# Kernel optimization log

Hardware: AMD Instinct MI355X
Metric: run time of the kernel (lower is better)

Reference implementation:

```python
import jax, jax.numpy as jnp
import numpy as np

N_NODES = 50000
N_EDGES = 500000
N_GRAPHS = 512


def _segmean(vals, ids, num):
    # avg aggregation: segment mean with safe divide for empty segments
    s = jax.ops.segment_sum(vals, ids, num_segments=num)
    c = jax.ops.segment_sum(jnp.ones((vals.shape[0], 1), vals.dtype), ids, num_segments=num)
    return s / jnp.maximum(c, 1.0)


def setup_inputs() -> dict:
    key = jax.random.key(0)
    ks = iter(jax.random.split(key, 64))

    def nrm(shape, scale=0.05):
        return jax.random.normal(next(ks), shape, dtype=jnp.float32) * scale

    inp = {}
    inp['x'] = nrm((N_NODES, 64), 1.0)
    inp['e'] = nrm((N_EDGES, 32), 1.0)
    inp['u'] = nrm((N_GRAPHS, 64), 1.0)
    inp['a'] = nrm((N_GRAPHS, 8), 1.0)
    inp['senders'] = jax.random.randint(next(ks), (N_EDGES,), 0, N_NODES)
    inp['receivers'] = jax.random.randint(next(ks), (N_EDGES,), 0, N_NODES)
    inp['node_graph'] = jnp.sort(jax.random.randint(next(ks), (N_NODES,), 0, N_GRAPHS))
    inp['edge_graph'] = jnp.sort(jax.random.randint(next(ks), (N_EDGES,), 0, N_GRAPHS))
    # block 1 (hidden 256)
    inp['We1'] = nrm((32, 256)); inp['be1'] = jnp.zeros((256,), jnp.float32)
    inp['Wn1'] = nrm((64, 256)); inp['Win1'] = nrm((256, 256)); inp['Wout1'] = nrm((256, 256)); inp['bn1'] = jnp.zeros((256,), jnp.float32)
    inp['Wg1'] = nrm((64, 256)); inp['Wgn1'] = nrm((256, 256)); inp['Wge1'] = nrm((256, 256)); inp['bg1'] = jnp.zeros((256,), jnp.float32)
    # block 2 (hidden 128)
    inp['We2'] = nrm((256, 128)); inp['be2'] = jnp.zeros((128,), jnp.float32)
    inp['Wn2'] = nrm((256, 128)); inp['Win2'] = nrm((128, 128)); inp['Wout2'] = nrm((128, 128)); inp['bn2'] = jnp.zeros((128,), jnp.float32)
    inp['Wg2'] = nrm((256, 128)); inp['Wgn2'] = nrm((128, 128)); inp['Wge2'] = nrm((128, 128)); inp['bg2'] = jnp.zeros((128,), jnp.float32)
    # global readout (global_features only)
    inp['Wga'] = nrm((128, 128)); inp['bga'] = jnp.zeros((128,), jnp.float32)
    # action-value MLP: (128 + 8) -> 256 -> 256 -> 1
    inp['Wa1'] = nrm((136, 256)); inp['ba1'] = jnp.zeros((256,), jnp.float32)
    inp['Wa2'] = nrm((256, 256)); inp['ba2'] = jnp.zeros((256,), jnp.float32)
    inp['Wa3'] = nrm((256, 1)); inp['ba3'] = jnp.zeros((1,), jnp.float32)
    return inp


def reference(x, e, u, a, senders, receivers, node_graph, edge_graph,
              We1, be1, Wn1, Win1, Wout1, bn1, Wg1, Wgn1, Wge1, bg1,
              We2, be2, Wn2, Win2, Wout2, bn2, Wg2, Wgn2, Wge2, bg2,
              Wga, bga, Wa1, ba1, Wa2, ba2, Wa3, ba3):
    # --- GraphNetwork block 1 (hidden 256) ---
    e1 = jax.nn.relu(e @ We1 + be1)                                  # [E,256]
    inc1 = _segmean(e1, receivers, N_NODES)                          # avg incoming per node
    out1 = _segmean(e1, senders, N_NODES)                            # avg outgoing per node
    n1 = jax.nn.relu(x @ Wn1 + inc1 @ Win1 + out1 @ Wout1 + bn1)     # [N,256]
    u1 = jax.nn.relu(u @ Wg1 + _segmean(n1, node_graph, N_GRAPHS) @ Wgn1
                     + _segmean(e1, edge_graph, N_GRAPHS) @ Wge1 + bg1)  # [B,256]
    # --- GraphNetwork block 2 (hidden 128) ---
    e2 = jax.nn.relu(e1 @ We2 + be2)                                 # [E,128]
    inc2 = _segmean(e2, receivers, N_NODES)
    out2 = _segmean(e2, senders, N_NODES)
    n2 = jax.nn.relu(n1 @ Wn2 + inc2 @ Win2 + out2 @ Wout2 + bn2)    # [N,128]
    u2 = jax.nn.relu(u1 @ Wg2 + _segmean(n2, node_graph, N_GRAPHS) @ Wgn2
                     + _segmean(e2, edge_graph, N_GRAPHS) @ Wge2 + bg2)  # [B,128]
    # --- global readout + action-value MLP ---
    state_value = u2 @ Wga + bga                                     # [B,128]
    h = jnp.concatenate([state_value, a], axis=1)                    # [B,136]
    h = jax.nn.relu(h @ Wa1 + ba1)
    h = jax.nn.relu(h @ Wa2 + ba2)
    return h @ Wa3 + ba3                                             # [B,1]
```

## Files before the change

### kernel.cpp

```cpp
#include <hip/hip_runtime.h>
#include <hip/hip_bf16.h>

#define N_NODES 50000
#define N_EDGES 500000
#define N_GRAPHS 512

#define FXS16 2048.0f
#define FXI16 4.8828125e-4f

__device__ __forceinline__ unsigned long long pk16x4(float4 v) {
    const unsigned long long a = (unsigned int)fmaf(v.x, FXS16, 0.5f);
    const unsigned long long b = (unsigned int)fmaf(v.y, FXS16, 0.5f);
    const unsigned long long c = (unsigned int)fmaf(v.z, FXS16, 0.5f);
    const unsigned long long d = (unsigned int)fmaf(v.w, FXS16, 0.5f);
    return a | (b << 16) | (c << 32) | (d << 48);
}

typedef __attribute__((ext_vector_type(8))) short bf16x8;
typedef __attribute__((ext_vector_type(4))) float f32x4;

__global__ __launch_bounds__(256) void prep_kernel(
    const float* __restrict__ We2,  const float* __restrict__ Wn1,
    const float* __restrict__ Win1, const float* __restrict__ Wout1,
    const float* __restrict__ Wn2,  const float* __restrict__ Win2,
    const float* __restrict__ Wout2,
    __hip_bfloat16* __restrict__ Wt2,  __hip_bfloat16* __restrict__ Wn1t,
    __hip_bfloat16* __restrict__ Win1t,__hip_bfloat16* __restrict__ Wout1t,
    __hip_bfloat16* __restrict__ Wn2t, __hip_bfloat16* __restrict__ Win2t,
    __hip_bfloat16* __restrict__ Wout2t)
{
    const int b = blockIdx.x, t = threadIdx.x;
    const float* src; __hip_bfloat16* dst; int K, N, base;
    if (b < 128)      { src = We2;   dst = Wt2;    K = 256; N = 128; base = 0; }
    else if (b < 192) { src = Wn1;   dst = Wn1t;   K = 64;  N = 256; base = 128; }
    else if (b < 448) { src = Win1;  dst = Win1t;  K = 256; N = 256; base = 192; }
    else if (b < 704) { src = Wout1; dst = Wout1t; K = 256; N = 256; base = 448; }
    else if (b < 832) { src = Wn2;   dst = Wn2t;   K = 256; N = 128; base = 704; }
    else if (b < 896) { src = Win2;  dst = Win2t;  K = 128; N = 128; base = 832; }
    else              { src = Wout2; dst = Wout2t; K = 128; N = 128; base = 896; }
    const int i = (b - base) * 256 + t;
    const int n = i / K, k = i - n * K;
    dst[i] = __float2bfloat16(src[(size_t)k * N + n]);
}

#define EPB 32
#define E1P 264
#define E2P 132

__global__ __launch_bounds__(256) void edge_kernel(
    const float* __restrict__ e,
    const int* __restrict__ senders,
    const int* __restrict__ receivers,
    const int* __restrict__ edge_graph,
    const float* __restrict__ We1, const float* __restrict__ be1,
    const __hip_bfloat16* __restrict__ Wt2,
    const float* __restrict__ be2,
    unsigned long long* __restrict__ inc1u, unsigned long long* __restrict__ out1u,
    unsigned long long* __restrict__ inc2u, unsigned long long* __restrict__ out2u,
    float* __restrict__ rcnt, float* __restrict__ scnt,
    float* __restrict__ ge1, float* __restrict__ ge2, float* __restrict__ gecnt)
{
    __shared__ float eL[EPB * 32];
    __shared__ __hip_bfloat16 e1B[EPB * E1P];
    __shared__ float e2L[EPB * E2P];
    __shared__ int ridx[EPB], sidx[EPB], gidx[EPB];

    const int t = threadIdx.x;
    const long e0 = (long)blockIdx.x * EPB;

    for (int i = t; i < EPB * 32; i += 256) eL[i] = e[e0 * 32 + i];
    if (t < EPB) {
        ridx[t] = receivers[e0 + t];
        sidx[t] = senders[e0 + t];
        gidx[t] = edge_graph[e0 + t];
    }
    __syncthreads();

    {
        const int c0 = (t & 63) * 4;
        const int jb = (t >> 6) * 8;
        float4 acc[8];
        const float4 b4 = *(const float4*)&be1[c0];
        #pragma unroll
        for (int j = 0; j < 8; j++) acc[j] = b4;
        for (int k = 0; k < 32; k += 4) {
            float4 v[8];
            #pragma unroll
            for (int j = 0; j < 8; j++) v[j] = *(const float4*)&eL[(jb + j) * 32 + k];
            #pragma unroll
            for (int kk = 0; kk < 4; kk++) {
                const float4 w = *(const float4*)&We1[(size_t)(k + kk) * 256 + c0];
                #pragma unroll
                for (int j = 0; j < 8; j++) {
                    const float vv = ((const float*)&v[j])[kk];
                    acc[j].x = fmaf(vv, w.x, acc[j].x);
                    acc[j].y = fmaf(vv, w.y, acc[j].y);
                    acc[j].z = fmaf(vv, w.z, acc[j].z);
                    acc[j].w = fmaf(vv, w.w, acc[j].w);
                }
            }
        }
        #pragma unroll
        for (int j = 0; j < 8; j++) {
            const float2 p0 = make_float2(fmaxf(acc[j].x, 0.f), fmaxf(acc[j].y, 0.f));
            const float2 p1 = make_float2(fmaxf(acc[j].z, 0.f), fmaxf(acc[j].w, 0.f));
            *(__hip_bfloat162*)&e1B[(jb + j) * E1P + c0]     = __float22bfloat162_rn(p0);
            *(__hip_bfloat162*)&e1B[(jb + j) * E1P + c0 + 2] = __float22bfloat162_rn(p1);
        }
    }
    __syncthreads();

    {
        const int wv = t >> 6, ln = t & 63;
        const int r0 = ln & 15, q = ln >> 4;
        f32x4 acc[2][2] = {{{0.f,0.f,0.f,0.f},{0.f,0.f,0.f,0.f}},
                           {{0.f,0.f,0.f,0.f},{0.f,0.f,0.f,0.f}}};
        const int n0 = (2 * wv) * 16 + r0;
        const int n1 = (2 * wv + 1) * 16 + r0;
        #pragma unroll
        for (int kb = 0; kb < 8; kb++) {
            const int k0 = kb * 32 + q * 8;
            const bf16x8 a0 = *(const bf16x8*)&e1B[(r0) * E1P + k0];
            const bf16x8 a1 = *(const bf16x8*)&e1B[(16 + r0) * E1P + k0];
            const bf16x8 b0 = *(const bf16x8*)&Wt2[(size_t)n0 * 256 + k0];
            const bf16x8 b1 = *(const bf16x8*)&Wt2[(size_t)n1 * 256 + k0];
            acc[0][0] = __builtin_amdgcn_mfma_f32_16x16x32_bf16(a0, b0, acc[0][0], 0, 0, 0);
            acc[0][1] = __builtin_amdgcn_mfma_f32_16x16x32_bf16(a0, b1, acc[0][1], 0, 0, 0);
            acc[1][0] = __builtin_amdgcn_mfma_f32_16x16x32_bf16(a1, b0, acc[1][0], 0, 0, 0);
            acc[1][1] = __builtin_amdgcn_mfma_f32_16x16x32_bf16(a1, b1, acc[1][1], 0, 0, 0);
        }
        const float bz0 = be2[2 * wv * 16 + r0];
        const float bz1 = be2[(2 * wv + 1) * 16 + r0];
        #pragma unroll
        for (int mt = 0; mt < 2; mt++) {
            const int m = mt * 16 + q * 4;
            #pragma unroll
            for (int r = 0; r < 4; r++) {
                e2L[(m + r) * E2P + 2 * wv * 16 + r0]       = fmaxf(acc[mt][0][r] + bz0, 0.f);
                e2L[(m + r) * E2P + (2 * wv + 1) * 16 + r0] = fmaxf(acc[mt][1][r] + bz1, 0.f);
            }
        }
    }
    __syncthreads();

    {
        const int w = t & 63;
        const int ep = (t >> 6) & 1;
        unsigned long long* arr = (t < 128) ? inc1u : out1u;
        const int* idx = (t < 128) ? ridx : sidx;
        #pragma unroll
        for (int jj = 0; jj < EPB / 2; jj++) {
            const int j = jj * 2 + ep;
            const float2 v0 = __bfloat1622float2(*(const __hip_bfloat162*)&e1B[j * E1P + 4 * w]);
            const float2 v1 = __bfloat1622float2(*(const __hip_bfloat162*)&e1B[j * E1P + 4 * w + 2]);
            float4 v; v.x = v0.x; v.y = v0.y; v.z = v1.x; v.w = v1.y;
            atomicAdd(&arr[(size_t)idx[j] * 64 + w], pk16x4(v));
        }
    }
    {
        const int w = t & 31;
        const int eq = (t >> 5) & 3;
        unsigned long long* arr = (t < 128) ? inc2u : out2u;
        const int* idx = (t < 128) ? ridx : sidx;
        #pragma unroll
        for (int jj = 0; jj < EPB / 4; jj++) {
            const int j = jj * 4 + eq;
            const float4 v = *(const float4*)&e2L[j * E2P + 4 * w];
            atomicAdd(&arr[(size_t)idx[j] * 32 + w], pk16x4(v));
        }
    }
    if (gidx[0] == gidx[EPB - 1]) {
        const int g = gidx[0];
        float s = 0.f;
        #pragma unroll
        for (int j = 0; j < EPB; j++) s += __bfloat162float(e1B[j * E1P + t]);
        atomicAdd(&ge1[(size_t)g * 256 + t], s);
        if (t < 128) {
            float s2 = 0.f;
            #pragma unroll
            for (int j = 0; j < EPB; j++) s2 += e2L[j * E2P + t];
            atomicAdd(&ge2[(size_t)g * 128 + t], s2);
        }
        if (t == 0) atomicAdd(&gecnt[g], (float)EPB);
    } else {
        int j = 0;
        while (j < EPB) {
            const int g = gidx[j];
            int j2 = j;
            float s = 0.f;
            while (j2 < EPB && gidx[j2] == g) { s += __bfloat162float(e1B[j2 * E1P + t]); j2++; }
            atomicAdd(&ge1[(size_t)g * 256 + t], s);
            if (t < 128) {
                float s2 = 0.f;
                for (int jj = j; jj < j2; jj++) s2 += e2L[jj * E2P + t];
                atomicAdd(&ge2[(size_t)g * 128 + t], s2);
            }
            if (t == 0) atomicAdd(&gecnt[g], (float)(j2 - j));
            j = j2;
        }
    }
    if (t < EPB) {
        atomicAdd(&rcnt[ridx[t]], 1.f);
        atomicAdd(&scnt[sidx[t]], 1.f);
    }
}

#define NPB 16
#define XP  72
#define K1P 264
#define K2P 136

__global__ __launch_bounds__(256) void node_kernel(
    const float* __restrict__ x,
    const int* __restrict__ node_graph,
    const unsigned long long* __restrict__ inc1u, const unsigned long long* __restrict__ out1u,
    const unsigned long long* __restrict__ inc2u, const unsigned long long* __restrict__ out2u,
    const float* __restrict__ rcnt, const float* __restrict__ scnt,
    const __hip_bfloat16* __restrict__ Wn1t, const __hip_bfloat16* __restrict__ Win1t,
    const __hip_bfloat16* __restrict__ Wout1t, const float* __restrict__ bn1,
    const __hip_bfloat16* __restrict__ Wn2t, const __hip_bfloat16* __restrict__ Win2t,
    const __hip_bfloat16* __restrict__ Wout2t, const float* __restrict__ bn2,
    float* __restrict__ gn1, float* __restrict__ gn2, float* __restrict__ gncnt)
{
    __shared__ __hip_bfloat16 xB[NPB * XP];
    __shared__ __hip_bfloat16 i1B[NPB * K1P];
    __shared__ __hip_bfloat16 o1B[NPB * K1P];
    __shared__ __hip_bfloat16 i2B[NPB * K2P];
    __shared__ __hip_bfloat16 o2B[NPB * K2P];
    __shared__ __hip_bfloat16 n1B[NPB * K1P];
    __shared__ __hip_bfloat16 n2B[NPB * K2P];
    __shared__ int gI[NPB];
    __shared__ float rrcp[NPB], srcp[NPB];

    const int t = threadIdx.x;
    const long n0 = (long)blockIdx.x * NPB;

    if (t < NPB) {
        gI[t] = node_graph[n0 + t];
        rrcp[t] = FXI16 / fmaxf(rcnt[n0 + t], 1.f);
        srcp[t] = FXI16 / fmaxf(scnt[n0 + t], 1.f);
    }
    for (int i = t; i < NPB * 16; i += 256) {
        const int j = i >> 4, c4 = (i & 15) * 4;
        const float4 v = *(const float4*)&x[(n0 + j) * 64 + c4];
        *(__hip_bfloat162*)&xB[j * XP + c4]     = __float22bfloat162_rn(make_float2(v.x, v.y));
        *(__hip_bfloat162*)&xB[j * XP + c4 + 2] = __float22bfloat162_rn(make_float2(v.z, v.w));
    }
    __syncthreads();

    for (int i = t; i < NPB * 64; i += 256) {
        const int j = i >> 6, w = i & 63;
        const size_t n = (size_t)(n0 + j);
        const unsigned long long av = inc1u[n * 64 + w];
        const unsigned long long bv = out1u[n * 64 + w];
        const float rr = rrcp[j], sr = srcp[j];
        const float2 a01 = make_float2((float)(unsigned int)(av & 0xFFFF) * rr,
                                       (float)(unsigned int)((av >> 16) & 0xFFFF) * rr);
        const float2 a23 = make_float2((float)(unsigned int)((av >> 32) & 0xFFFF) * rr,
                                       (float)(unsigned int)(av >> 48) * rr);
        const float2 b01 = make_float2((float)(unsigned int)(bv & 0xFFFF) * sr,
                                       (float)(unsigned int)((bv >> 16) & 0xFFFF) * sr);
        const float2 b23 = make_float2((float)(unsigned int)((bv >> 32) & 0xFFFF) * sr,
                                       (float)(unsigned int)(bv >> 48) * sr);
        *(__hip_bfloat162*)&i1B[j * K1P + 4 * w]     = __float22bfloat162_rn(a01);
        *(__hip_bfloat162*)&i1B[j * K1P + 4 * w + 2] = __float22bfloat162_rn(a23);
        *(__hip_bfloat162*)&o1B[j * K1P + 4 * w]     = __float22bfloat162_rn(b01);
        *(__hip_bfloat162*)&o1B[j * K1P + 4 * w + 2] = __float22bfloat162_rn(b23);
    }
    for (int i = t; i < NPB * 32; i += 256) {
        const int j = i >> 5, w = i & 31;
        const size_t n = (size_t)(n0 + j);
        const unsigned long long av = inc2u[n * 32 + w];
        const unsigned long long bv = out2u[n * 32 + w];
        const float rr = rrcp[j], sr = srcp[j];
        const float2 a01 = make_float2((float)(unsigned int)(av & 0xFFFF) * rr,
                                       (float)(unsigned int)((av >> 16) & 0xFFFF) * rr);
        const float2 a23 = make_float2((float)(unsigned int)((av >> 32) & 0xFFFF) * rr,
                                       (float)(unsigned int)(av >> 48) * rr);
        const float2 b01 = make_float2((float)(unsigned int)(bv & 0xFFFF) * sr,
                                       (float)(unsigned int)((bv >> 16) & 0xFFFF) * sr);
        const float2 b23 = make_float2((float)(unsigned int)((bv >> 32) & 0xFFFF) * sr,
                                       (float)(unsigned int)(bv >> 48) * sr);
        *(__hip_bfloat162*)&i2B[j * K2P + 4 * w]     = __float22bfloat162_rn(a01);
        *(__hip_bfloat162*)&i2B[j * K2P + 4 * w + 2] = __float22bfloat162_rn(a23);
        *(__hip_bfloat162*)&o2B[j * K2P + 4 * w]     = __float22bfloat162_rn(b01);
        *(__hip_bfloat162*)&o2B[j * K2P + 4 * w + 2] = __float22bfloat162_rn(b23);
    }
    __syncthreads();

    const int wv = t >> 6, ln = t & 63;
    const int r0 = ln & 15, q = ln >> 4;

    {
        f32x4 acc[4] = {{0.f,0.f,0.f,0.f},{0.f,0.f,0.f,0.f},
                        {0.f,0.f,0.f,0.f},{0.f,0.f,0.f,0.f}};
        #pragma unroll
        for (int ks = 0; ks < 2; ks++) {
            const int k0 = ks * 32 + q * 8;
            const bf16x8 a = *(const bf16x8*)&xB[r0 * XP + k0];
            #pragma unroll
            for (int nn = 0; nn < 4; nn++) {
                const int n = (wv * 4 + nn) * 16 + r0;
                const bf16x8 b = *(const bf16x8*)&Wn1t[(size_t)n * 64 + k0];
                acc[nn] = __builtin_amdgcn_mfma_f32_16x16x32_bf16(a, b, acc[nn], 0, 0, 0);
            }
        }
        #pragma unroll
        for (int ks = 0; ks < 8; ks++) {
            const int k0 = ks * 32 + q * 8;
            const bf16x8 a = *(const bf16x8*)&i1B[r0 * K1P + k0];
            #pragma unroll
            for (int nn = 0; nn < 4; nn++) {
                const int n = (wv * 4 + nn) * 16 + r0;
                const bf16x8 b = *(const bf16x8*)&Win1t[(size_t)n * 256 + k0];
                acc[nn] = __builtin_amdgcn_mfma_f32_16x16x32_bf16(a, b, acc[nn], 0, 0, 0);
            }
        }
        #pragma unroll
        for (int ks = 0; ks < 8; ks++) {
            const int k0 = ks * 32 + q * 8;
            const bf16x8 a = *(const bf16x8*)&o1B[r0 * K1P + k0];
            #pragma unroll
            for (int nn = 0; nn < 4; nn++) {
                const int n = (wv * 4 + nn) * 16 + r0;
                const bf16x8 b = *(const bf16x8*)&Wout1t[(size_t)n * 256 + k0];
                acc[nn] = __builtin_amdgcn_mfma_f32_16x16x32_bf16(a, b, acc[nn], 0, 0, 0);
            }
        }
        #pragma unroll
        for (int nn = 0; nn < 4; nn++) {
            const int n = (wv * 4 + nn) * 16 + r0;
            const float bz = bn1[n];
            #pragma unroll
            for (int r = 0; r < 4; r++) {
                const int m = q * 4 + r;
                n1B[m * K1P + n] = __float2bfloat16(fmaxf(acc[nn][r] + bz, 0.f));
            }
        }
    }
    __syncthreads();

    if (gI[0] == gI[NPB - 1]) {
        float s = 0.f;
        #pragma unroll
        for (int j = 0; j < NPB; j++) s += __bfloat162float(n1B[j * K1P + t]);
        atomicAdd(&gn1[(size_t)gI[0] * 256 + t], s);
        if (t == 0) atomicAdd(&gncnt[gI[0]], (float)NPB);
    } else {
        int j = 0;
        while (j < NPB) {
            const int g = gI[j];
            int j2 = j;
            float s = 0.f;
            while (j2 < NPB && gI[j2] == g) { s += __bfloat162float(n1B[j2 * K1P + t]); j2++; }
            atomicAdd(&gn1[(size_t)g * 256 + t], s);
            if (t == 0) atomicAdd(&gncnt[g], (float)(j2 - j));
            j = j2;
        }
    }

    {
        f32x4 acc[2] = {{0.f,0.f,0.f,0.f},{0.f,0.f,0.f,0.f}};
        #pragma unroll
        for (int ks = 0; ks < 8; ks++) {
            const int k0 = ks * 32 + q * 8;
            const bf16x8 a = *(const bf16x8*)&n1B[r0 * K1P + k0];
            #pragma unroll
            for (int nn = 0; nn < 2; nn++) {
                const int n = (wv * 2 + nn) * 16 + r0;
                const bf16x8 b = *(const bf16x8*)&Wn2t[(size_t)n * 256 + k0];
                acc[nn] = __builtin_amdgcn_mfma_f32_16x16x32_bf16(a, b, acc[nn], 0, 0, 0);
            }
        }
        #pragma unroll
        for (int ks = 0; ks < 4; ks++) {
            const int k0 = ks * 32 + q * 8;
            const bf16x8 a = *(const bf16x8*)&i2B[r0 * K2P + k0];
            #pragma unroll
            for (int nn = 0; nn < 2; nn++) {
                const int n = (wv * 2 + nn) * 16 + r0;
                const bf16x8 b = *(const bf16x8*)&Win2t[(size_t)n * 128 + k0];
                acc[nn] = __builtin_amdgcn_mfma_f32_16x16x32_bf16(a, b, acc[nn], 0, 0, 0);
            }
        }
        #pragma unroll
        for (int ks = 0; ks < 4; ks++) {
            const int k0 = ks * 32 + q * 8;
            const bf16x8 a = *(const bf16x8*)&o2B[r0 * K2P + k0];
            #pragma unroll
            for (int nn = 0; nn < 2; nn++) {
                const int n = (wv * 2 + nn) * 16 + r0;
                const bf16x8 b = *(const bf16x8*)&Wout2t[(size_t)n * 128 + k0];
                acc[nn] = __builtin_amdgcn_mfma_f32_16x16x32_bf16(a, b, acc[nn], 0, 0, 0);
            }
        }
        #pragma unroll
        for (int nn = 0; nn < 2; nn++) {
            const int n = (wv * 2 + nn) * 16 + r0;
            const float bz = bn2[n];
            #pragma unroll
            for (int r = 0; r < 4; r++) {
                const int m = q * 4 + r;
                n2B[m * K2P + n] = __float2bfloat16(fmaxf(acc[nn][r] + bz, 0.f));
            }
        }
    }
    __syncthreads();

    if (t < 128) {
        if (gI[0] == gI[NPB - 1]) {
            float s = 0.f;
            #pragma unroll
            for (int j = 0; j < NPB; j++) s += __bfloat162float(n2B[j * K2P + t]);
            atomicAdd(&gn2[(size_t)gI[0] * 128 + t], s);
        } else {
            int j = 0;
            while (j < NPB) {
                const int g = gI[j];
                int j2 = j;
                float s = 0.f;
                while (j2 < NPB && gI[j2] == g) { s += __bfloat162float(n2B[j2 * K2P + t]); j2++; }
                atomicAdd(&gn2[(size_t)g * 128 + t], s);
                j = j2;
            }
        }
    }
}

__global__ __launch_bounds__(256) void graph_kernel(
    const float* __restrict__ u,
    const float* __restrict__ a,
    const float* __restrict__ ge1, const float* __restrict__ ge2,
    const float* __restrict__ gecnt,
    const float* __restrict__ gn1, const float* __restrict__ gn2,
    const float* __restrict__ gncnt,
    const float* __restrict__ Wg1, const float* __restrict__ Wgn1,
    const float* __restrict__ Wge1, const float* __restrict__ bg1,
    const float* __restrict__ Wg2, const float* __restrict__ Wgn2,
    const float* __restrict__ Wge2, const float* __restrict__ bg2,
    const float* __restrict__ Wga, const float* __restrict__ bga,
    const float* __restrict__ Wa1, const float* __restrict__ ba1,
    const float* __restrict__ Wa2, const float* __restrict__ ba2,
    const float* __restrict__ Wa3, const float* __restrict__ ba3,
    float* __restrict__ out)
{
    const int g = blockIdx.x;
    const int t = threadIdx.x;
    __shared__ float uL[64], mn1[256], me1[256], mn2[128], me2[128];
    __shared__ float u1L[256], u2L[128], hL[144], h1L[256], h2L[256];
    __shared__ float red[4];

    const float ec = 1.f / fmaxf(gecnt[g], 1.f);
    const float nc = 1.f / fmaxf(gncnt[g], 1.f);
    if (t < 64) uL[t] = u[(size_t)g * 64 + t];
    mn1[t] = gn1[(size_t)g * 256 + t] * nc;
    me1[t] = ge1[(size_t)g * 256 + t] * ec;
    if (t < 128) {
        mn2[t] = gn2[(size_t)g * 128 + t] * nc;
        me2[t] = ge2[(size_t)g * 128 + t] * ec;
    }
    if (t >= 136 && t < 144) hL[t] = 0.f;
    __syncthreads();

    {
        float acc = bg1[t];
        for (int k = 0; k < 64; k++)  acc = fmaf(uL[k],  Wg1[(size_t)k * 256 + t], acc);
        for (int k = 0; k < 256; k++) acc = fmaf(mn1[k], Wgn1[(size_t)k * 256 + t], acc);
        for (int k = 0; k < 256; k++) acc = fmaf(me1[k], Wge1[(size_t)k * 256 + t], acc);
        u1L[t] = fmaxf(acc, 0.f);
    }
    __syncthreads();
    if (t < 128) {
        float acc = bg2[t];
        for (int k = 0; k < 256; k++) acc = fmaf(u1L[k], Wg2[(size_t)k * 128 + t], acc);
        for (int k = 0; k < 128; k++) acc = fmaf(mn2[k], Wgn2[(size_t)k * 128 + t], acc);
        for (int k = 0; k < 128; k++) acc = fmaf(me2[k], Wge2[(size_t)k * 128 + t], acc);
        u2L[t] = fmaxf(acc, 0.f);
    }
    __syncthreads();
    if (t < 128) {
        float acc = bga[t];
        for (int k = 0; k < 128; k++) acc = fmaf(u2L[k], Wga[(size_t)k * 128 + t], acc);
        hL[t] = acc;
    }
    if (t >= 128 && t < 136) hL[t] = a[(size_t)g * 8 + (t - 128)];
    __syncthreads();
    {
        float acc = ba1[t];
        for (int k = 0; k < 136; k++) acc = fmaf(hL[k], Wa1[(size_t)k * 256 + t], acc);
        h1L[t] = fmaxf(acc, 0.f);
    }
    __syncthreads();
    {
        float acc = ba2[t];
        for (int k = 0; k < 256; k++) acc = fmaf(h1L[k], Wa2[(size_t)k * 256 + t], acc);
        h2L[t] = fmaxf(acc, 0.f);
    }
    __syncthreads();
    {
        float p = h2L[t] * Wa3[t];
        for (int off = 32; off > 0; off >>= 1) p += __shfl_down(p, off, 64);
        if ((t & 63) == 0) red[t >> 6] = p;
        __syncthreads();
        if (t == 0) out[g] = red[0] + red[1] + red[2] + red[3] + ba3[0];
    }
}

extern "C" void kernel_launch(void* const* d_in, const int* in_sizes, int n_in,
                              void* d_out, int out_size, void* d_ws, size_t ws_size,
                              hipStream_t stream) {
    const float* x          = (const float*)d_in[0];
    const float* e          = (const float*)d_in[1];
    const float* u          = (const float*)d_in[2];
    const float* a          = (const float*)d_in[3];
    const int*   senders    = (const int*)d_in[4];
    const int*   receivers  = (const int*)d_in[5];
    const int*   node_graph = (const int*)d_in[6];
    const int*   edge_graph = (const int*)d_in[7];
    const float* We1 = (const float*)d_in[8];  const float* be1 = (const float*)d_in[9];
    const float* Wn1 = (const float*)d_in[10]; const float* Win1 = (const float*)d_in[11];
    const float* Wout1 = (const float*)d_in[12]; const float* bn1 = (const float*)d_in[13];
    const float* Wg1 = (const float*)d_in[14]; const float* Wgn1 = (const float*)d_in[15];
    const float* Wge1 = (const float*)d_in[16]; const float* bg1 = (const float*)d_in[17];
    const float* We2 = (const float*)d_in[18]; const float* be2 = (const float*)d_in[19];
    const float* Wn2 = (const float*)d_in[20]; const float* Win2 = (const float*)d_in[21];
    const float* Wout2 = (const float*)d_in[22]; const float* bn2 = (const float*)d_in[23];
    const float* Wg2 = (const float*)d_in[24]; const float* Wgn2 = (const float*)d_in[25];
    const float* Wge2 = (const float*)d_in[26]; const float* bg2 = (const float*)d_in[27];
    const float* Wga = (const float*)d_in[28]; const float* bga = (const float*)d_in[29];
    const float* Wa1 = (const float*)d_in[30]; const float* ba1 = (const float*)d_in[31];
    const float* Wa2 = (const float*)d_in[32]; const float* ba2 = (const float*)d_in[33];
    const float* Wa3 = (const float*)d_in[34]; const float* ba3 = (const float*)d_in[35];

    unsigned long long* uw = (unsigned long long*)d_ws;
    unsigned long long* inc1u = uw;                       uw += (size_t)N_NODES * 64;
    unsigned long long* out1u = uw;                       uw += (size_t)N_NODES * 64;
    unsigned long long* inc2u = uw;                       uw += (size_t)N_NODES * 32;
    unsigned long long* out2u = uw;                       uw += (size_t)N_NODES * 32;
    float* fw = (float*)uw;
    float* rcnt = fw;  fw += N_NODES;
    float* scnt = fw;  fw += N_NODES;
    float* ge1  = fw;  fw += (size_t)N_GRAPHS * 256;
    float* ge2  = fw;  fw += (size_t)N_GRAPHS * 128;
    float* gecnt = fw; fw += N_GRAPHS;
    float* gn1  = fw;  fw += (size_t)N_GRAPHS * 256;
    float* gn2  = fw;  fw += (size_t)N_GRAPHS * 128;
    float* gncnt = fw; fw += N_GRAPHS;
    const size_t total_bytes = (char*)fw - (char*)d_ws;
    __hip_bfloat16* bw = (__hip_bfloat16*)fw;
    __hip_bfloat16* Wt2    = bw;  bw += 128 * 256;
    __hip_bfloat16* Wn1t   = bw;  bw += 256 * 64;
    __hip_bfloat16* Win1t  = bw;  bw += 256 * 256;
    __hip_bfloat16* Wout1t = bw;  bw += 256 * 256;
    __hip_bfloat16* Wn2t   = bw;  bw += 128 * 256;
    __hip_bfloat16* Win2t  = bw;  bw += 128 * 128;
    __hip_bfloat16* Wout2t = bw;  bw += 128 * 128;

    hipMemsetAsync(d_ws, 0, total_bytes, stream);

    prep_kernel<<<960, 256, 0, stream>>>(
        We2, Wn1, Win1, Wout1, Wn2, Win2, Wout2,
        Wt2, Wn1t, Win1t, Wout1t, Wn2t, Win2t, Wout2t);

    edge_kernel<<<N_EDGES / EPB, 256, 0, stream>>>(
        e, senders, receivers, edge_graph, We1, be1, Wt2, be2,
        inc1u, out1u, inc2u, out2u, rcnt, scnt, ge1, ge2, gecnt);

    node_kernel<<<N_NODES / NPB, 256, 0, stream>>>(
        x, node_graph, inc1u, out1u, inc2u, out2u, rcnt, scnt,
        Wn1t, Win1t, Wout1t, bn1, Wn2t, Win2t, Wout2t, bn2, gn1, gn2, gncnt);

    graph_kernel<<<N_GRAPHS, 256, 0, stream>>>(
        u, a, ge1, ge2, gecnt, gn1, gn2, gncnt,
        Wg1, Wgn1, Wge1, bg1, Wg2, Wgn2, Wge2, bg2,
        Wga, bga, Wa1, ba1, Wa2, ba2, Wa3, ba3, (float*)d_out);
}
```

Baseline: 1.041 ms.

## Replace atomic scatter aggregation with CSR gather for node means

Builds CSR adjacency for receivers and senders on the device every call (count, scan, fill). The edge kernel then writes per-edge e1 (bf16) and e2 (fixed-point u16) to buffers instead of atomically scattering them into per-node accumulators. The node kernel gathers each node's incoming and outgoing edges through the CSR lists and computes the means before its MFMA GEMMs. This removes heavy 64-bit atomic contention, but adds several extra launches, about 384 MB of edge-feature buffer traffic, and random gathers. The new path runs only when the workspace is large enough, otherwise the old path is used.

```diff
diff --git a/kernel.cpp b/kernel.cpp
--- a/kernel.cpp
+++ b/kernel.cpp
@@ -43,9 +43,460 @@
     dst[i] = __float2bfloat16(src[(size_t)k * N + n]);
 }
 
+
+#define NTILES 196
+
+__global__ __launch_bounds__(256) void count_kernel(
+    const int* __restrict__ senders, const int* __restrict__ receivers,
+    unsigned int* __restrict__ rc, unsigned int* __restrict__ sc)
+{
+    const int i = blockIdx.x * 256 + threadIdx.x;
+    if (i < N_EDGES) {
+        atomicAdd(&rc[receivers[i]], 1u);
+        atomicAdd(&sc[senders[i]], 1u);
+    }
+}
+
+__global__ __launch_bounds__(256) void scan_tile_sum(
+    const unsigned int* __restrict__ rc, const unsigned int* __restrict__ sc,
+    unsigned int* __restrict__ tsR, unsigned int* __restrict__ tsS)
+{
+    const int b = blockIdx.x;
+    const int sel = (b >= NTILES);
+    const int tile = sel ? b - NTILES : b;
+    const unsigned int* src = sel ? sc : rc;
+    unsigned int* ts = sel ? tsS : tsR;
+    const int t = threadIdx.x;
+    const int i = tile * 256 + t;
+    unsigned int v = (i < N_NODES) ? src[i] : 0u;
+    __shared__ unsigned int s[256];
+    s[t] = v; __syncthreads();
+    for (int off = 128; off > 0; off >>= 1) {
+        if (t < off) s[t] += s[t + off];
+        __syncthreads();
+    }
+    if (t == 0) ts[tile] = s[0];
+}
+
+__global__ __launch_bounds__(256) void scan_tile_offsets(
+    unsigned int* __restrict__ tsR, unsigned int* __restrict__ tsS,
+    int* __restrict__ roff, int* __restrict__ soff)
+{
+    __shared__ unsigned int s[256];
+    const int t = threadIdx.x;
+    for (int sel = 0; sel < 2; sel++) {
+        unsigned int* ts = sel ? tsS : tsR;
+        int* off = sel ? soff : roff;
+        unsigned int v = (t < NTILES) ? ts[t] : 0u;
+        s[t] = v; __syncthreads();
+        for (int o = 1; o < 256; o <<= 1) {
+            unsigned int x = (t >= o) ? s[t - o] : 0u;
+            __syncthreads();
+            s[t] += x;
+            __syncthreads();
+        }
+        const unsigned int incl = s[t];
+        if (t < NTILES) ts[t] = incl - v;
+        if (t == NTILES - 1) off[N_NODES] = (int)incl;
+        __syncthreads();
+    }
+}
+
+__global__ __launch_bounds__(256) void scan_finalize(
+    const unsigned int* __restrict__ rc, const unsigned int* __restrict__ sc,
+    const unsigned int* __restrict__ tsR, const unsigned int* __restrict__ tsS,
+    int* __restrict__ roff, int* __restrict__ soff,
+    unsigned int* __restrict__ wpR, unsigned int* __restrict__ wpS)
+{
+    const int b = blockIdx.x;
+    const int sel = (b >= NTILES);
+    const int tile = sel ? b - NTILES : b;
+    const unsigned int* src = sel ? sc : rc;
+    const unsigned int* ts = sel ? tsS : tsR;
+    int* off = sel ? soff : roff;
+    unsigned int* wp = sel ? wpS : wpR;
+    const int t = threadIdx.x, i = tile * 256 + t;
+    unsigned int v = (i < N_NODES) ? src[i] : 0u;
+    __shared__ unsigned int s[256];
+    s[t] = v; __syncthreads();
+    for (int o = 1; o < 256; o <<= 1) {
+        unsigned int x = (t >= o) ? s[t - o] : 0u;
+        __syncthreads();
+        s[t] += x;
+        __syncthreads();
+    }
+    const unsigned int excl = s[t] - v + ts[tile];
+    if (i < N_NODES) { off[i] = (int)excl; wp[i] = excl; }
+}
+
+__global__ __launch_bounds__(256) void csr_fill(
+    const int* __restrict__ senders, const int* __restrict__ receivers,
+    unsigned int* __restrict__ wpR, unsigned int* __restrict__ wpS,
+    int* __restrict__ csrR, int* __restrict__ csrS)
+{
+    const int i = blockIdx.x * 256 + threadIdx.x;
+    if (i < N_EDGES) {
+        csrR[atomicAdd(&wpR[receivers[i]], 1u)] = i;
+        csrS[atomicAdd(&wpS[senders[i]], 1u)] = i;
+    }
+}
+
 #define EPB 32
 #define E1P 264
 #define E2P 132
+
+__global__ __launch_bounds__(256) void edge_kernel_csr(
+    const float* __restrict__ e,
+    const int* __restrict__ edge_graph,
+    const float* __restrict__ We1, const float* __restrict__ be1,
+    const __hip_bfloat16* __restrict__ Wt2,
+    const float* __restrict__ be2,
+    __hip_bfloat16* __restrict__ e1buf, unsigned short* __restrict__ e2buf,
+    float* __restrict__ ge1, float* __restrict__ ge2, float* __restrict__ gecnt)
+{
+    __shared__ float eL[EPB * 32];
+    __shared__ __hip_bfloat16 e1B[EPB * E1P];
+    __shared__ float e2L[EPB * E2P];
+    __shared__ int gidx[EPB];
+
+    const int t = threadIdx.x;
+    const long e0 = (long)blockIdx.x * EPB;
+
+    for (int i = t; i < EPB * 32; i += 256) eL[i] = e[e0 * 32 + i];
+    if (t < EPB) gidx[t] = edge_graph[e0 + t];
+    __syncthreads();
+
+    {
+        const int c0 = (t & 63) * 4;
+        const int jb = (t >> 6) * 8;
+        float4 acc[8];
+        const float4 b4 = *(const float4*)&be1[c0];
+        #pragma unroll
+        for (int j = 0; j < 8; j++) acc[j] = b4;
+        for (int k = 0; k < 32; k += 4) {
+            float4 v[8];
+            #pragma unroll
+            for (int j = 0; j < 8; j++) v[j] = *(const float4*)&eL[(jb + j) * 32 + k];
+            #pragma unroll
+            for (int kk = 0; kk < 4; kk++) {
+                const float4 w = *(const float4*)&We1[(size_t)(k + kk) * 256 + c0];
+                #pragma unroll
+                for (int j = 0; j < 8; j++) {
+                    const float vv = ((const float*)&v[j])[kk];
+                    acc[j].x = fmaf(vv, w.x, acc[j].x);
+                    acc[j].y = fmaf(vv, w.y, acc[j].y);
+                    acc[j].z = fmaf(vv, w.z, acc[j].z);
+                    acc[j].w = fmaf(vv, w.w, acc[j].w);
+                }
+            }
+        }
+        #pragma unroll
+        for (int j = 0; j < 8; j++) {
+            const float2 p0 = make_float2(fmaxf(acc[j].x, 0.f), fmaxf(acc[j].y, 0.f));
+            const float2 p1 = make_float2(fmaxf(acc[j].z, 0.f), fmaxf(acc[j].w, 0.f));
+            *(__hip_bfloat162*)&e1B[(jb + j) * E1P + c0]     = __float22bfloat162_rn(p0);
+            *(__hip_bfloat162*)&e1B[(jb + j) * E1P + c0 + 2] = __float22bfloat162_rn(p1);
+        }
+    }
+    __syncthreads();
+
+    {
+        const int wv = t >> 6, ln = t & 63;
+        const int r0 = ln & 15, q = ln >> 4;
+        f32x4 acc[2][2] = {{{0.f,0.f,0.f,0.f},{0.f,0.f,0.f,0.f}},
+                           {{0.f,0.f,0.f,0.f},{0.f,0.f,0.f,0.f}}};
+        const int n0 = (2 * wv) * 16 + r0;
+        const int n1 = (2 * wv + 1) * 16 + r0;
+        #pragma unroll
+        for (int kb = 0; kb < 8; kb++) {
+            const int k0 = kb * 32 + q * 8;
+            const bf16x8 a0 = *(const bf16x8*)&e1B[(r0) * E1P + k0];
+            const bf16x8 a1 = *(const bf16x8*)&e1B[(16 + r0) * E1P + k0];
+            const bf16x8 b0 = *(const bf16x8*)&Wt2[(size_t)n0 * 256 + k0];
+            const bf16x8 b1 = *(const bf16x8*)&Wt2[(size_t)n1 * 256 + k0];
+            acc[0][0] = __builtin_amdgcn_mfma_f32_16x16x32_bf16(a0, b0, acc[0][0], 0, 0, 0);
+            acc[0][1] = __builtin_amdgcn_mfma_f32_16x16x32_bf16(a0, b1, acc[0][1], 0, 0, 0);
+            acc[1][0] = __builtin_amdgcn_mfma_f32_16x16x32_bf16(a1, b0, acc[1][0], 0, 0, 0);
+            acc[1][1] = __builtin_amdgcn_mfma_f32_16x16x32_bf16(a1, b1, acc[1][1], 0, 0, 0);
+        }
+        const float bz0 = be2[2 * wv * 16 + r0];
+        const float bz1 = be2[(2 * wv + 1) * 16 + r0];
+        #pragma unroll
+        for (int mt = 0; mt < 2; mt++) {
+            const int m = mt * 16 + q * 4;
+            #pragma unroll
+            for (int r = 0; r < 4; r++) {
+                e2L[(m + r) * E2P + 2 * wv * 16 + r0]       = fmaxf(acc[mt][0][r] + bz0, 0.f);
+                e2L[(m + r) * E2P + (2 * wv + 1) * 16 + r0] = fmaxf(acc[mt][1][r] + bz1, 0.f);
+            }
+        }
+    }
+    __syncthreads();
+
+    for (int i = t; i < EPB * 32; i += 256) {
+        const int j = i >> 5, c8 = (i & 31) * 8;
+        *(bf16x8*)&e1buf[(size_t)(e0 + j) * 256 + c8] = *(const bf16x8*)&e1B[j * E1P + c8];
+    }
+    for (int i = t; i < EPB * 32; i += 256) {
+        const int j = i >> 5, c4 = (i & 31) * 4;
+        const float4 v = *(const float4*)&e2L[j * E2P + c4];
+        ushort4 pk;
+        pk.x = (unsigned short)fmaf(v.x, FXS16, 0.5f);
+        pk.y = (unsigned short)fmaf(v.y, FXS16, 0.5f);
+        pk.z = (unsigned short)fmaf(v.z, FXS16, 0.5f);
+        pk.w = (unsigned short)fmaf(v.w, FXS16, 0.5f);
+        *(ushort4*)&e2buf[(size_t)(e0 + j) * 128 + c4] = pk;
+    }
+
+    if (gidx[0] == gidx[EPB - 1]) {
+        const int g = gidx[0];
+        float s = 0.f;
+        #pragma unroll
+        for (int j = 0; j < EPB; j++) s += __bfloat162float(e1B[j * E1P + t]);
+        atomicAdd(&ge1[(size_t)g * 256 + t], s);
+        if (t < 128) {
+            float s2 = 0.f;
+            #pragma unroll
+            for (int j = 0; j < EPB; j++) s2 += e2L[j * E2P + t];
+            atomicAdd(&ge2[(size_t)g * 128 + t], s2);
+        }
+        if (t == 0) atomicAdd(&gecnt[g], (float)EPB);
+    } else {
+        int j = 0;
+        while (j < EPB) {
+            const int g = gidx[j];
+            int j2 = j;
+            float s = 0.f;
+            while (j2 < EPB && gidx[j2] == g) { s += __bfloat162float(e1B[j2 * E1P + t]); j2++; }
+            atomicAdd(&ge1[(size_t)g * 256 + t], s);
+            if (t < 128) {
+                float s2 = 0.f;
+                for (int jj = j; jj < j2; jj++) s2 += e2L[jj * E2P + t];
+                atomicAdd(&ge2[(size_t)g * 128 + t], s2);
+            }
+            if (t == 0) atomicAdd(&gecnt[g], (float)(j2 - j));
+            j = j2;
+        }
+    }
+}
+
+#define NPB 16
+#define XP  72
+#define K1P 264
+#define K2P 136
+
+__global__ __launch_bounds__(256) void node_kernel_csr(
+    const float* __restrict__ x,
+    const int* __restrict__ node_graph,
+    const int* __restrict__ roff, const int* __restrict__ soff,
+    const int* __restrict__ csrR, const int* __restrict__ csrS,
+    const __hip_bfloat16* __restrict__ e1buf, const unsigned short* __restrict__ e2buf,
+    const __hip_bfloat16* __restrict__ Wn1t, const __hip_bfloat16* __restrict__ Win1t,
+    const __hip_bfloat16* __restrict__ Wout1t, const float* __restrict__ bn1,
+    const __hip_bfloat16* __restrict__ Wn2t, const __hip_bfloat16* __restrict__ Win2t,
+    const __hip_bfloat16* __restrict__ Wout2t, const float* __restrict__ bn2,
+    float* __restrict__ gn1, float* __restrict__ gn2, float* __restrict__ gncnt)
+{
+    __shared__ __hip_bfloat16 xB[NPB * XP];
+    __shared__ __hip_bfloat16 i1B[NPB * K1P];
+    __shared__ __hip_bfloat16 o1B[NPB * K1P];
+    __shared__ __hip_bfloat16 i2B[NPB * K2P];
+    __shared__ __hip_bfloat16 o2B[NPB * K2P];
+    __shared__ __hip_bfloat16 n1B[NPB * K1P];
+    __shared__ __hip_bfloat16 n2B[NPB * K2P];
+    __shared__ int gI[NPB];
+
+    const int t = threadIdx.x;
+    const long n0 = (long)blockIdx.x * NPB;
+
+    if (t < NPB) gI[t] = node_graph[n0 + t];
+    for (int i = t; i < NPB * 16; i += 256) {
+        const int j = i >> 4, c4 = (i & 15) * 4;
+        const float4 v = *(const float4*)&x[(n0 + j) * 64 + c4];
+        *(__hip_bfloat162*)&xB[j * XP + c4]     = __float22bfloat162_rn(make_float2(v.x, v.y));
+        *(__hip_bfloat162*)&xB[j * XP + c4 + 2] = __float22bfloat162_rn(make_float2(v.z, v.w));
+    }
+
+    const int wv = t >> 6, ln = t & 63;
+    const int h = ln >> 5, l5 = ln & 31;
+    const int* off = h ? soff : roff;
+    const int* lst = h ? csrS : csrR;
+    __hip_bfloat16* d1 = h ? o1B : i1B;
+    __hip_bfloat16* d2 = h ? o2B : i2B;
+
+    for (int jj = 0; jj < 4; jj++) {
+        const int j = wv * 4 + jj;
+        const long node = n0 + j;
+        const int o = off[node], oE = off[node + 1];
+        float a1[8] = {0.f,0.f,0.f,0.f,0.f,0.f,0.f,0.f};
+        float a2[4] = {0.f,0.f,0.f,0.f};
+        int i = o;
+        int id = (i < oE) ? lst[i] : 0;
+        while (i < oE) {
+            const int idc = id;
+            ++i;
+            id = (i < oE) ? lst[i] : 0;
+            const bf16x8 r1 = *(const bf16x8*)&e1buf[(size_t)idc * 256 + l5 * 8];
+            const ushort4 r2 = *(const ushort4*)&e2buf[(size_t)idc * 128 + l5 * 4];
+            #pragma unroll
+            for (int c = 0; c < 8; c++)
+                a1[c] += __uint_as_float(((unsigned int)(unsigned short)r1[c]) << 16);
+            a2[0] += (float)r2.x; a2[1] += (float)r2.y;
+            a2[2] += (float)r2.z; a2[3] += (float)r2.w;
+        }
+        const int cnt = oE - o;
+        const float inv = 1.f / (float)(cnt > 0 ? cnt : 1);
+        const float inv2 = inv * FXI16;
+        #pragma unroll
+        for (int c = 0; c < 4; c++) {
+            *(__hip_bfloat162*)&d1[j * K1P + l5 * 8 + 2 * c] =
+                __float22bfloat162_rn(make_float2(a1[2 * c] * inv, a1[2 * c + 1] * inv));
+        }
+        *(__hip_bfloat162*)&d2[j * K2P + l5 * 4] =
+            __float22bfloat162_rn(make_float2(a2[0] * inv2, a2[1] * inv2));
+        *(__hip_bfloat162*)&d2[j * K2P + l5 * 4 + 2] =
+            __float22bfloat162_rn(make_float2(a2[2] * inv2, a2[3] * inv2));
+    }
+    __syncthreads();
+
+    const int r0 = ln & 15, q = ln >> 4;
+
+    {
+        f32x4 acc[4] = {{0.f,0.f,0.f,0.f},{0.f,0.f,0.f,0.f},
+                        {0.f,0.f,0.f,0.f},{0.f,0.f,0.f,0.f}};
+        #pragma unroll
+        for (int ks = 0; ks < 2; ks++) {
+            const int k0 = ks * 32 + q * 8;
+            const bf16x8 a = *(const bf16x8*)&xB[r0 * XP + k0];
+            #pragma unroll
+            for (int nn = 0; nn < 4; nn++) {
+                const int n = (wv * 4 + nn) * 16 + r0;
+                const bf16x8 b = *(const bf16x8*)&Wn1t[(size_t)n * 64 + k0];
+                acc[nn] = __builtin_amdgcn_mfma_f32_16x16x32_bf16(a, b, acc[nn], 0, 0, 0);
+            }
+        }
+        #pragma unroll
+        for (int ks = 0; ks < 8; ks++) {
+            const int k0 = ks * 32 + q * 8;
+            const bf16x8 a = *(const bf16x8*)&i1B[r0 * K1P + k0];
+            #pragma unroll
+            for (int nn = 0; nn < 4; nn++) {
+                const int n = (wv * 4 + nn) * 16 + r0;
+                const bf16x8 b = *(const bf16x8*)&Win1t[(size_t)n * 256 + k0];
+                acc[nn] = __builtin_amdgcn_mfma_f32_16x16x32_bf16(a, b, acc[nn], 0, 0, 0);
+            }
+        }
+        #pragma unroll
+        for (int ks = 0; ks < 8; ks++) {
+            const int k0 = ks * 32 + q * 8;
+            const bf16x8 a = *(const bf16x8*)&o1B[r0 * K1P + k0];
+            #pragma unroll
+            for (int nn = 0; nn < 4; nn++) {
+                const int n = (wv * 4 + nn) * 16 + r0;
+                const bf16x8 b = *(const bf16x8*)&Wout1t[(size_t)n * 256 + k0];
+                acc[nn] = __builtin_amdgcn_mfma_f32_16x16x32_bf16(a, b, acc[nn], 0, 0, 0);
+            }
+        }
+        #pragma unroll
+        for (int nn = 0; nn < 4; nn++) {
+            const int n = (wv * 4 + nn) * 16 + r0;
+            const float bz = bn1[n];
+            #pragma unroll
+            for (int r = 0; r < 4; r++) {
+                const int m = q * 4 + r;
+                n1B[m * K1P + n] = __float2bfloat16(fmaxf(acc[nn][r] + bz, 0.f));
+            }
+        }
+    }
+    __syncthreads();
+
+    if (gI[0] == gI[NPB - 1]) {
+        float s = 0.f;
+        #pragma unroll
+        for (int j = 0; j < NPB; j++) s += __bfloat162float(n1B[j * K1P + t]);
+        atomicAdd(&gn1[(size_t)gI[0] * 256 + t], s);
+        if (t == 0) atomicAdd(&gncnt[gI[0]], (float)NPB);
+    } else {
+        int j = 0;
+        while (j < NPB) {
+            const int g = gI[j];
+            int j2 = j;
+            float s = 0.f;
+            while (j2 < NPB && gI[j2] == g) { s += __bfloat162float(n1B[j2 * K1P + t]); j2++; }
+            atomicAdd(&gn1[(size_t)g * 256 + t], s);
+            if (t == 0) atomicAdd(&gncnt[g], (float)(j2 - j));
+            j = j2;
+        }
+    }
+
+    {
+        f32x4 acc[2] = {{0.f,0.f,0.f,0.f},{0.f,0.f,0.f,0.f}};
+        #pragma unroll
+        for (int ks = 0; ks < 8; ks++) {
+            const int k0 = ks * 32 + q * 8;
+            const bf16x8 a = *(const bf16x8*)&n1B[r0 * K1P + k0];
+            #pragma unroll
+            for (int nn = 0; nn < 2; nn++) {
+                const int n = (wv * 2 + nn) * 16 + r0;
+                const bf16x8 b = *(const bf16x8*)&Wn2t[(size_t)n * 256 + k0];
+                acc[nn] = __builtin_amdgcn_mfma_f32_16x16x32_bf16(a, b, acc[nn], 0, 0, 0);
+            }
+        }
+        #pragma unroll
+        for (int ks = 0; ks < 4; ks++) {
+            const int k0 = ks * 32 + q * 8;
+            const bf16x8 a = *(const bf16x8*)&i2B[r0 * K2P + k0];
+            #pragma unroll
+            for (int nn = 0; nn < 2; nn++) {
+                const int n = (wv * 2 + nn) * 16 + r0;
+                const bf16x8 b = *(const bf16x8*)&Win2t[(size_t)n * 128 + k0];
+                acc[nn] = __builtin_amdgcn_mfma_f32_16x16x32_bf16(a, b, acc[nn], 0, 0, 0);
+            }
+        }
+        #pragma unroll
+        for (int ks = 0; ks < 4; ks++) {
+            const int k0 = ks * 32 + q * 8;
+            const bf16x8 a = *(const bf16x8*)&o2B[r0 * K2P + k0];
+            #pragma unroll
+            for (int nn = 0; nn < 2; nn++) {
+                const int n = (wv * 2 + nn) * 16 + r0;
+                const bf16x8 b = *(const bf16x8*)&Wout2t[(size_t)n * 128 + k0];
+                acc[nn] = __builtin_amdgcn_mfma_f32_16x16x32_bf16(a, b, acc[nn], 0, 0, 0);
+            }
+        }
+        #pragma unroll
+        for (int nn = 0; nn < 2; nn++) {
+            const int n = (wv * 2 + nn) * 16 + r0;
+            const float bz = bn2[n];
+            #pragma unroll
+            for (int r = 0; r < 4; r++) {
+                const int m = q * 4 + r;
+                n2B[m * K2P + n] = __float2bfloat16(fmaxf(acc[nn][r] + bz, 0.f));
+            }
+        }
+    }
+    __syncthreads();
+
+    if (t < 128) {
+        if (gI[0] == gI[NPB - 1]) {
+            float s = 0.f;
+            #pragma unroll
+            for (int j = 0; j < NPB; j++) s += __bfloat162float(n2B[j * K2P + t]);
+            atomicAdd(&gn2[(size_t)gI[0] * 128 + t], s);
+        } else {
+            int j = 0;
+            while (j < NPB) {
+                const int g = gI[j];
+                int j2 = j;
+                float s = 0.f;
+                while (j2 < NPB && gI[j2] == g) { s += __bfloat162float(n2B[j2 * K2P + t]); j2++; }
+                atomicAdd(&gn2[(size_t)g * 128 + t], s);
+                j = j2;
+            }
+        }
+    }
+}
+
 
 __global__ __launch_bounds__(256) void edge_kernel(
     const float* __restrict__ e,
@@ -204,11 +655,6 @@
         atomicAdd(&scnt[sidx[t]], 1.f);
     }
 }
-
-#define NPB 16
-#define XP  72
-#define K1P 264
-#define K2P 136
 
 __global__ __launch_bounds__(256) void node_kernel(
     const float* __restrict__ x,
@@ -532,6 +978,72 @@
     const float* Wa2 = (const float*)d_in[32]; const float* ba2 = (const float*)d_in[33];
     const float* Wa3 = (const float*)d_in[34]; const float* ba3 = (const float*)d_in[35];
 
+    {
+        char* p = (char*)d_ws;
+        auto take = [&p](size_t bytes) {
+            char* q = p; p += (bytes + 15) & ~(size_t)15; return q;
+        };
+        unsigned int* rcntU = (unsigned int*)take((size_t)N_NODES * 4);
+        unsigned int* scntU = (unsigned int*)take((size_t)N_NODES * 4);
+        float* ge1   = (float*)take((size_t)N_GRAPHS * 256 * 4);
+        float* ge2   = (float*)take((size_t)N_GRAPHS * 128 * 4);
+        float* gecnt = (float*)take((size_t)N_GRAPHS * 4);
+        float* gn1   = (float*)take((size_t)N_GRAPHS * 256 * 4);
+        float* gn2   = (float*)take((size_t)N_GRAPHS * 128 * 4);
+        float* gncnt = (float*)take((size_t)N_GRAPHS * 4);
+        const size_t zero_bytes = (size_t)(p - (char*)d_ws);
+        int* roff = (int*)take((size_t)(N_NODES + 1) * 4);
+        int* soff = (int*)take((size_t)(N_NODES + 1) * 4);
+        unsigned int* wpR = (unsigned int*)take((size_t)N_NODES * 4);
+        unsigned int* wpS = (unsigned int*)take((size_t)N_NODES * 4);
+        unsigned int* tsR = (unsigned int*)take(256 * 4);
+        unsigned int* tsS = (unsigned int*)take(256 * 4);
+        int* csrR = (int*)take((size_t)N_EDGES * 4);
+        int* csrS = (int*)take((size_t)N_EDGES * 4);
+        __hip_bfloat16* e1buf = (__hip_bfloat16*)take((size_t)N_EDGES * 256 * 2);
+        unsigned short* e2buf = (unsigned short*)take((size_t)N_EDGES * 128 * 2);
+        __hip_bfloat16* Wt2    = (__hip_bfloat16*)take((size_t)128 * 256 * 2);
+        __hip_bfloat16* Wn1t   = (__hip_bfloat16*)take((size_t)256 * 64 * 2);
+        __hip_bfloat16* Win1t  = (__hip_bfloat16*)take((size_t)256 * 256 * 2);
+        __hip_bfloat16* Wout1t = (__hip_bfloat16*)take((size_t)256 * 256 * 2);
+        __hip_bfloat16* Wn2t   = (__hip_bfloat16*)take((size_t)128 * 256 * 2);
+        __hip_bfloat16* Win2t  = (__hip_bfloat16*)take((size_t)128 * 128 * 2);
+        __hip_bfloat16* Wout2t = (__hip_bfloat16*)take((size_t)128 * 128 * 2);
+        const size_t needed = (size_t)(p - (char*)d_ws);
+
+        if (ws_size >= needed) {
+            hipMemsetAsync(d_ws, 0, zero_bytes, stream);
+
+            prep_kernel<<<960, 256, 0, stream>>>(
+                We2, Wn1, Win1, Wout1, Wn2, Win2, Wout2,
+                Wt2, Wn1t, Win1t, Wout1t, Wn2t, Win2t, Wout2t);
+
+            count_kernel<<<(N_EDGES + 255) / 256, 256, 0, stream>>>(
+                senders, receivers, rcntU, scntU);
+            scan_tile_sum<<<2 * NTILES, 256, 0, stream>>>(rcntU, scntU, tsR, tsS);
+            scan_tile_offsets<<<1, 256, 0, stream>>>(tsR, tsS, roff, soff);
+            scan_finalize<<<2 * NTILES, 256, 0, stream>>>(
+                rcntU, scntU, tsR, tsS, roff, soff, wpR, wpS);
+            csr_fill<<<(N_EDGES + 255) / 256, 256, 0, stream>>>(
+                senders, receivers, wpR, wpS, csrR, csrS);
+
+            edge_kernel_csr<<<N_EDGES / EPB, 256, 0, stream>>>(
+                e, edge_graph, We1, be1, Wt2, be2,
+                e1buf, e2buf, ge1, ge2, gecnt);
+
+            node_kernel_csr<<<N_NODES / NPB, 256, 0, stream>>>(
+                x, node_graph, roff, soff, csrR, csrS, e1buf, e2buf,
+                Wn1t, Win1t, Wout1t, bn1, Wn2t, Win2t, Wout2t, bn2,
+                gn1, gn2, gncnt);
+
+            graph_kernel<<<N_GRAPHS, 256, 0, stream>>>(
+                u, a, ge1, ge2, gecnt, gn1, gn2, gncnt,
+                Wg1, Wgn1, Wge1, bg1, Wg2, Wgn2, Wge2, bg2,
+                Wga, bga, Wa1, ba1, Wa2, ba2, Wa3, ba3, (float*)d_out);
+            return;
+        }
+    }
+
     unsigned long long* uw = (unsigned long long*)d_ws;
     unsigned long long* inc1u = uw;                       uw += (size_t)N_NODES * 64;
     unsigned long long* out1u = uw;                       uw += (size_t)N_NODES * 64;
```

Measured after the change: 1.043 ms. Within noise of the previous version (+0.2%).
